# Optimization experiments

Hardware: AMD Instinct MI355X
Metric: run time of the kernel (lower is better)

Reference implementation:

```python
import jax, jax.numpy as jnp
import numpy as np
from jax import lax

B, C, H, W = 8, 128, 256, 256
OUT_CH = 64
IN_CH = C * 9  # 1152: module's in_channels = 9 * image channels (unfold with 3x3 kernel)


def setup_inputs() -> dict:
    key = jax.random.key(0)
    k1, k2, k3 = jax.random.split(key, 3)
    x = jax.random.normal(k1, (B, C, H, W), dtype=jnp.float32)
    style = jax.random.normal(k2, (B, IN_CH), dtype=jnp.float32)
    # learned parameter: torch.randn(out_channels, in_channels, 1, 1) -> store as (out, in)
    weight = jax.random.normal(k3, (OUT_CH, IN_CH), dtype=jnp.float32)
    return {"x": x, "style": style, "weight": weight}


def reference(x, style, weight):
    b, c, h, w = x.shape
    out_ch, in_ch = weight.shape  # in_ch == c * 9
    # unfold column ordering is (c, kh, kw), so the flattened weight is exactly a
    # 3x3 conv kernel: (out, c*9) -> (out, c, 3, 3)
    w33 = weight.reshape(out_ch, c, 3, 3)
    # style.view(B,1,in_ch,1,1) * weight -> per-sample modulated 3x3 kernels
    w_mod = style.reshape(b, 1, c, 3, 3) * w33[None]  # (B, out, c, 3, 3)

    def conv_one(xi, wi):
        # xi: (c, h, w), wi: (out, c, 3, 3); SAME padding matches padding=(1,1)
        return lax.conv_general_dilated(
            xi[None], wi, window_strides=(1, 1), padding="SAME",
            dimension_numbers=("NCHW", "OIHW", "NCHW"))[0]

    out = jax.vmap(conv_one)(x, w_mod)  # (B, out, h, w)
    return out
```

## Files before the change

kernel.cpp:

```cpp
#include <hip/hip_runtime.h>
#include <hip/hip_bf16.h>

#define BATCH 8
#define CIN   128
#define HH    256
#define WW    256
#define OUTC  64
#define INCH  1152
#define HW    (HH*WW)

typedef __attribute__((ext_vector_type(8))) short short8;
typedef __attribute__((ext_vector_type(4))) float f32x4;

__device__ __forceinline__ unsigned short bf16r(float f) {
    unsigned u = __builtin_bit_cast(unsigned, f);
    u += 0x7fffu + ((u >> 16) & 1u);
    return (unsigned short)(u >> 16);
}

__global__ void __launch_bounds__(256) wmod_kernel(const float* __restrict__ weight,
                                                   const float* __restrict__ style,
                                                   unsigned short* __restrict__ wmod) {
    int i = blockIdx.x * 256 + threadIdx.x;
    if (i >= BATCH * 9 * OUTC * CIN) return;
    int c    = i & (CIN - 1);
    int rest = i >> 7;
    int o    = rest & (OUTC - 1);
    int bt   = rest >> 6;
    int tap  = bt % 9;
    int b    = bt / 9;
    int k    = c * 9 + tap;
    float v = weight[o * INCH + k] * style[b * INCH + k];
    wmod[i] = bf16r(v);
}

template <bool GW>
__global__ void __launch_bounds__(512, 4) conv_kernel(
    const float* __restrict__ x,
    const unsigned short* __restrict__ wmod,
    const float* __restrict__ weight,
    const float* __restrict__ style,
    float* __restrict__ out)
{
    __shared__ __align__(16) unsigned short xs_sm[170 * 64];

    const int tid = threadIdx.x;
    const int bx  = blockIdx.x;
    const int b   = blockIdx.y;
    const int h0  = (bx >> 3) * 8;
    const int w0  = (bx & 7) * 32;

    const int wv  = tid >> 6;
    const int wr  = wv >> 2;
    const int wc  = wv & 3;
    const int l15 = tid & 15;
    const int kg  = (tid >> 4) & 3;

    int sbase[4];
#pragma unroll
    for (int ni = 0; ni < 4; ++ni) {
        int p = wc * 64 + ni * 16 + l15;
        sbase[ni] = (p >> 5) * 34 + (p & 31);
    }

    const bool tvalid = tid < 400;
    const int scg = tvalid ? tid / 100 : 0;
    const int srw = tvalid ? tid % 100 : 0;
    const int sr  = srw / 10;
    const int swq = srw % 10;
    const int sh  = h0 - 1 + sr;
    const bool hok = (unsigned)sh < HH;
    const int wload  = w0 - 4 + swq * 4;
    const int wclamp = min(max(wload, 0), WW - 4);
    const int gbase  = (hok ? sh : 0) * WW + wclamp;

    f32x4 acc[2][4];
#pragma unroll
    for (int mi = 0; mi < 2; ++mi)
#pragma unroll
        for (int ni = 0; ni < 4; ++ni) acc[mi][ni] = (f32x4){0.f, 0.f, 0.f, 0.f};

    for (int chunk = 0; chunk < 4; ++chunk) {
        if (chunk) __syncthreads();

        if (tvalid) {
            const float* xp =
                x + ((size_t)(b * CIN + chunk * 32 + scg * 8)) * HW + gbase;
            f32x4 f[8];
#pragma unroll
            for (int j = 0; j < 8; ++j)
                f[j] = hok ? *(const f32x4*)(xp + (size_t)j * HW)
                           : (f32x4){0.f, 0.f, 0.f, 0.f};
#pragma unroll
            for (int u = 0; u < 4; ++u) {
                int w   = wload + u;
                int col = w - (w0 - 1);
                if (col >= 0 && col <= 33) {
                    bool wok = hok && ((unsigned)w < WW);
                    short8 sv;
#pragma unroll
                    for (int j = 0; j < 8; ++j)
                        sv[j] = wok ? (short)bf16r(f[j][u]) : (short)0;
                    int s = sr * 34 + col;
                    int q = s >> 1;
                    int g = (((s & 1) << 2) | scg) ^ (q & 7);
                    *(short8*)&xs_sm[q * 64 + g * 8] = sv;
                }
            }
        }
        __syncthreads();

        const unsigned short* wmb = wmod + ((size_t)(b * 9) * OUTC) * CIN + chunk * 32;
#pragma unroll
        for (int tap = 0; tap < 9; ++tap) {
            const int kh = tap / 3, kw = tap % 3;

            short8 A[2];
            if (GW) {
                const unsigned short* wt = wmb + (size_t)tap * OUTC * CIN;
#pragma unroll
                for (int mi = 0; mi < 2; ++mi)
                    A[mi] = *(const short8*)(wt + (wr * 32 + mi * 16 + l15) * CIN +
                                             kg * 8);
            } else {
#pragma unroll
                for (int mi = 0; mi < 2; ++mi) {
                    int o = wr * 32 + mi * 16 + l15;
#pragma unroll
                    for (int j = 0; j < 8; ++j) {
                        int c = chunk * 32 + kg * 8 + j;
                        int k = c * 9 + tap;
                        A[mi][j] = (short)bf16r(weight[o * INCH + k] *
                                                style[b * INCH + k]);
                    }
                }
            }

            short8 Bv[4];
#pragma unroll
            for (int ni = 0; ni < 4; ++ni) {
                int s = sbase[ni] + kh * 34 + kw;
                int q = s >> 1;
                int g = (((s & 1) << 2) | kg) ^ (q & 7);
                Bv[ni] = *(const short8*)&xs_sm[q * 64 + g * 8];
            }
#pragma unroll
            for (int mi = 0; mi < 2; ++mi)
#pragma unroll
                for (int ni = 0; ni < 4; ++ni)
                    acc[mi][ni] = __builtin_amdgcn_mfma_f32_16x16x32_bf16(
                        A[mi], Bv[ni], acc[mi][ni], 0, 0, 0);
        }
    }

    float* op = out + ((size_t)b * OUTC) * HW;
#pragma unroll
    for (int mi = 0; mi < 2; ++mi) {
#pragma unroll
        for (int ni = 0; ni < 4; ++ni) {
            int p = wc * 64 + ni * 16 + l15;
            int h = h0 + (p >> 5), w = w0 + (p & 31);
#pragma unroll
            for (int r = 0; r < 4; ++r) {
                int o = wr * 32 + mi * 16 + kg * 4 + r;
                op[(size_t)o * HW + h * WW + w] = acc[mi][ni][r];
            }
        }
    }
}

extern "C" void kernel_launch(void* const* d_in, const int* in_sizes, int n_in,
                              void* d_out, int out_size, void* d_ws, size_t ws_size,
                              hipStream_t stream) {
    const float* x      = (const float*)d_in[0];
    const float* style  = (const float*)d_in[1];
    const float* weight = (const float*)d_in[2];
    float* out = (float*)d_out;

    const size_t wmod_bytes = (size_t)BATCH * 9 * OUTC * CIN * sizeof(unsigned short);
    if (ws_size >= wmod_bytes) {
        int total = BATCH * 9 * OUTC * CIN;
        wmod_kernel<<<(total + 255) / 256, 256, 0, stream>>>(weight, style,
                                                             (unsigned short*)d_ws);
        conv_kernel<true><<<dim3(256, BATCH), 512, 0, stream>>>(
            x, (const unsigned short*)d_ws, nullptr, nullptr, out);
    } else {
        conv_kernel<false><<<dim3(256, BATCH), 512, 0, stream>>>(
            x, nullptr, weight, style, out);
    }
}
```

Baseline: 227.4 us.

## Pre-transpose input to NHWC bf16 and double-buffer LDS with async global-to-LDS loads

Result: slower. 327.9 us (+44.2%).

```diff
diff --git a/kernel.cpp b/kernel.cpp
--- a/kernel.cpp
+++ b/kernel.cpp
@@ -9,13 +9,26 @@
 #define INCH  1152
 #define HW    (HH*WW)
 
+#define XT_BYTES   ((size_t)BATCH * HH * WW * CIN * 2)
+#define WMOD_BYTES ((size_t)BATCH * 9 * OUTC * CIN * 2)
+#define ZG_BYTES   16
+
 typedef __attribute__((ext_vector_type(8))) short short8;
 typedef __attribute__((ext_vector_type(4))) float f32x4;
+typedef __attribute__((ext_vector_type(4))) unsigned int u32x4;
 
 __device__ __forceinline__ unsigned short bf16r(float f) {
     unsigned u = __builtin_bit_cast(unsigned, f);
     u += 0x7fffu + ((u >> 16) & 1u);
     return (unsigned short)(u >> 16);
+}
+
+__device__ __forceinline__ void gload_lds16(const unsigned short* src,
+                                            unsigned short* dst_lds) {
+    __builtin_amdgcn_global_load_lds(
+        (const __attribute__((address_space(1))) unsigned int*)(const void*)src,
+        (__attribute__((address_space(3))) unsigned int*)(void*)dst_lds,
+        16, 0, 0);
 }
 
 __global__ void __launch_bounds__(256) wmod_kernel(const float* __restrict__ weight,
@@ -34,6 +47,154 @@
     wmod[i] = bf16r(v);
 }
 
+__global__ void __launch_bounds__(256) transpose_kernel(const float* __restrict__ x,
+                                                        unsigned short* __restrict__ xT) {
+    const int w  = blockIdx.x * 64 + (threadIdx.x & 63);
+    const int c0 = (threadIdx.x >> 6) * 32;
+    const int h  = blockIdx.y;
+    const int b  = blockIdx.z;
+
+    const float* xp = x + ((size_t)(b * CIN + c0)) * HW + h * WW + w;
+    unsigned short* op = xT + ((size_t)(b * HH + h) * WW + w) * CIN + c0;
+
+    float f[32];
+#pragma unroll
+    for (int j = 0; j < 32; ++j) f[j] = xp[(size_t)j * HW];
+
+    unsigned pk[16];
+#pragma unroll
+    for (int j = 0; j < 16; ++j)
+        pk[j] = (unsigned)bf16r(f[2 * j]) | ((unsigned)bf16r(f[2 * j + 1]) << 16);
+
+#pragma unroll
+    for (int u = 0; u < 4; ++u) {
+        u32x4 v = {pk[u * 4 + 0], pk[u * 4 + 1], pk[u * 4 + 2], pk[u * 4 + 3]};
+        *(u32x4*)(op + u * 8) = v;
+    }
+}
+
+__global__ void __launch_bounds__(512, 4) conv2_kernel(
+    const unsigned short* __restrict__ xT,
+    const unsigned short* __restrict__ wmod,
+    const unsigned short* __restrict__ zerog,
+    float* __restrict__ out)
+{
+    __shared__ __align__(16) unsigned short xs_sm[2][170 * 64];
+
+    const int tid = threadIdx.x;
+    const int bx  = blockIdx.x;
+    const int b   = blockIdx.y;
+    const int h0  = (bx >> 3) * 8;
+    const int w0  = (bx & 7) * 32;
+
+    const int wv  = tid >> 6;
+    const int wr  = wv >> 2;
+    const int wc  = wv & 3;
+    const int l15 = tid & 15;
+    const int kg  = (tid >> 4) & 3;
+
+    size_t goff[3];
+    bool   gok[3];
+#pragma unroll
+    for (int i = 0; i < 3; ++i) {
+        int G = tid + i * 512;
+        int Gc = (G < 1360) ? G : 0;
+        int q = Gc >> 3, g = Gc & 7;
+        int pc = g ^ (q & 7);
+        int s  = (q << 1) | (pc >> 2);
+        int cg = pc & 3;
+        int r   = s / 34;
+        int col = s - r * 34;
+        int h = h0 - 1 + r, w = w0 - 1 + col;
+        gok[i]  = ((unsigned)h < HH) && ((unsigned)w < WW);
+        goff[i] = ((size_t)(b * HH + (h & 255)) * WW + (w & 255)) * CIN + cg * 8;
+    }
+
+    int sbase[4];
+#pragma unroll
+    for (int ni = 0; ni < 4; ++ni) {
+        int p = wc * 64 + ni * 16 + l15;
+        sbase[ni] = (p >> 5) * 34 + (p & 31);
+    }
+
+    f32x4 acc[2][4];
+#pragma unroll
+    for (int mi = 0; mi < 2; ++mi)
+#pragma unroll
+        for (int ni = 0; ni < 4; ++ni) acc[mi][ni] = (f32x4){0.f, 0.f, 0.f, 0.f};
+
+    auto stage = [&](int chunk, unsigned short* buf) {
+#pragma unroll
+        for (int i = 0; i < 3; ++i) {
+            if (i < 2 || tid < 336) {
+                const unsigned short* src =
+                    gok[i] ? (xT + goff[i] + chunk * 32) : zerog;
+                unsigned short* dst = buf + (i * 512 + wv * 64) * 8;
+                gload_lds16(src, dst);
+            }
+        }
+    };
+
+    auto compute = [&](int chunk, const unsigned short* xs) {
+        const unsigned short* wmb =
+            wmod + ((size_t)(b * 9) * OUTC) * CIN + chunk * 32;
+#pragma unroll
+        for (int tap = 0; tap < 9; ++tap) {
+            const int kh = tap / 3, kw = tap % 3;
+
+            short8 A[2];
+            const unsigned short* wt = wmb + (size_t)tap * OUTC * CIN;
+#pragma unroll
+            for (int mi = 0; mi < 2; ++mi)
+                A[mi] = *(const short8*)(wt + (wr * 32 + mi * 16 + l15) * CIN +
+                                         kg * 8);
+
+            short8 Bv[4];
+#pragma unroll
+            for (int ni = 0; ni < 4; ++ni) {
+                int s = sbase[ni] + kh * 34 + kw;
+                int q = s >> 1;
+                int g = (((s & 1) << 2) | kg) ^ (q & 7);
+                Bv[ni] = *(const short8*)&xs[q * 64 + g * 8];
+            }
+#pragma unroll
+            for (int mi = 0; mi < 2; ++mi)
+#pragma unroll
+                for (int ni = 0; ni < 4; ++ni)
+                    acc[mi][ni] = __builtin_amdgcn_mfma_f32_16x16x32_bf16(
+                        A[mi], Bv[ni], acc[mi][ni], 0, 0, 0);
+        }
+    };
+
+    stage(0, xs_sm[0]);
+    __syncthreads();
+    stage(1, xs_sm[1]);
+    compute(0, xs_sm[0]);
+    __syncthreads();
+    stage(2, xs_sm[0]);
+    compute(1, xs_sm[1]);
+    __syncthreads();
+    stage(3, xs_sm[1]);
+    compute(2, xs_sm[0]);
+    __syncthreads();
+    compute(3, xs_sm[1]);
+
+    float* op = out + ((size_t)b * OUTC) * HW;
+#pragma unroll
+    for (int mi = 0; mi < 2; ++mi) {
+#pragma unroll
+        for (int ni = 0; ni < 4; ++ni) {
+            int p = wc * 64 + ni * 16 + l15;
+            int h = h0 + (p >> 5), w = w0 + (p & 31);
+#pragma unroll
+            for (int r = 0; r < 4; ++r) {
+                int o = wr * 32 + mi * 16 + kg * 4 + r;
+                op[(size_t)o * HW + h * WW + w] = acc[mi][ni][r];
+            }
+        }
+    }
+}
+
 template <bool GW>
 __global__ void __launch_bounds__(512, 4) conv_kernel(
     const float* __restrict__ x,
@@ -177,13 +338,22 @@
     const float* weight = (const float*)d_in[2];
     float* out = (float*)d_out;
 
-    const size_t wmod_bytes = (size_t)BATCH * 9 * OUTC * CIN * sizeof(unsigned short);
-    if (ws_size >= wmod_bytes) {
-        int total = BATCH * 9 * OUTC * CIN;
-        wmod_kernel<<<(total + 255) / 256, 256, 0, stream>>>(weight, style,
-                                                             (unsigned short*)d_ws);
+    const int wmod_total = BATCH * 9 * OUTC * CIN;
+
+    if (ws_size >= XT_BYTES + WMOD_BYTES + ZG_BYTES) {
+        unsigned short* xT    = (unsigned short*)d_ws;
+        unsigned short* wmodp = (unsigned short*)((char*)d_ws + XT_BYTES);
+        unsigned short* zerog = (unsigned short*)((char*)d_ws + XT_BYTES + WMOD_BYTES);
+
+        wmod_kernel<<<(wmod_total + 255) / 256, 256, 0, stream>>>(weight, style, wmodp);
+        transpose_kernel<<<dim3(4, HH, BATCH), 256, 0, stream>>>(x, xT);
+        hipMemsetAsync(zerog, 0, ZG_BYTES, stream);
+        conv2_kernel<<<dim3(256, BATCH), 512, 0, stream>>>(xT, wmodp, zerog, out);
+    } else if (ws_size >= WMOD_BYTES) {
+        unsigned short* wmodp = (unsigned short*)d_ws;
+        wmod_kernel<<<(wmod_total + 255) / 256, 256, 0, stream>>>(weight, style, wmodp);
         conv_kernel<true><<<dim3(256, BATCH), 512, 0, stream>>>(
-            x, (const unsigned short*)d_ws, nullptr, nullptr, out);
+            x, wmodp, nullptr, nullptr, out);
     } else {
         conv_kernel<false><<<dim3(256, BATCH), 512, 0, stream>>>(
             x, nullptr, weight, style, out);
```

## Shrink conv tiles and double-buffer LDS with register-prefetched input chunks

Applied to the files above, without the earlier changes.

New measurement: 264.3 us. +16.2%, slower.

```diff
diff --git a/kernel.cpp b/kernel.cpp
--- a/kernel.cpp
+++ b/kernel.cpp
@@ -8,9 +8,11 @@
 #define OUTC  64
 #define INCH  1152
 #define HW    (HH*WW)
+#define WMOD_BYTES ((size_t)BATCH * 9 * OUTC * CIN * 2)
 
 typedef __attribute__((ext_vector_type(8))) short short8;
 typedef __attribute__((ext_vector_type(4))) float f32x4;
+typedef __attribute__((ext_vector_type(4), aligned(4))) float f32x4u;
 
 __device__ __forceinline__ unsigned short bf16r(float f) {
     unsigned u = __builtin_bit_cast(unsigned, f);
@@ -30,49 +32,48 @@
     int tap  = bt % 9;
     int b    = bt / 9;
     int k    = c * 9 + tap;
-    float v = weight[o * INCH + k] * style[b * INCH + k];
-    wmod[i] = bf16r(v);
+    wmod[i] = bf16r(weight[o * INCH + k] * style[b * INCH + k]);
 }
 
 template <bool GW>
-__global__ void __launch_bounds__(512, 4) conv_kernel(
+__global__ void __launch_bounds__(128, 2) conv4_kernel(
     const float* __restrict__ x,
     const unsigned short* __restrict__ wmod,
     const float* __restrict__ weight,
     const float* __restrict__ style,
     float* __restrict__ out)
 {
-    __shared__ __align__(16) unsigned short xs_sm[170 * 64];
+    __shared__ __align__(16) unsigned short xs_sm[2][108 * 32];
 
     const int tid = threadIdx.x;
     const int bx  = blockIdx.x;
     const int b   = blockIdx.y;
-    const int h0  = (bx >> 3) * 8;
-    const int w0  = (bx & 7) * 32;
-
-    const int wv  = tid >> 6;
-    const int wr  = wv >> 2;
-    const int wc  = wv & 3;
+    const int h0  = (bx >> 4) * 4;
+    const int w0  = (bx & 15) * 16;
+
+    const int wr  = tid >> 6;
     const int l15 = tid & 15;
     const int kg  = (tid >> 4) & 3;
 
-    int sbase[4];
-#pragma unroll
-    for (int ni = 0; ni < 4; ++ni) {
-        int p = wc * 64 + ni * 16 + l15;
-        sbase[ni] = (p >> 5) * 34 + (p & 31);
+    {
+        short8 z = {0, 0, 0, 0, 0, 0, 0, 0};
+        short8* p = (short8*)&xs_sm[0][0];
+        for (int i = tid; i < 2 * 108 * 32 / 8; i += 128) p[i] = z;
     }
 
-    const bool tvalid = tid < 400;
-    const int scg = tvalid ? tid / 100 : 0;
-    const int srw = tvalid ? tid % 100 : 0;
-    const int sr  = srw / 10;
-    const int swq = srw % 10;
+    const bool tval = tid < 120;
+    const int tt  = tval ? tid : 0;
+    const int cg  = tt / 30;
+    const int rem = tt % 30;
+    const int sr  = rem / 5;
+    const int wq  = rem % 5;
     const int sh  = h0 - 1 + sr;
-    const bool hok = (unsigned)sh < HH;
-    const int wload  = w0 - 4 + swq * 4;
-    const int wclamp = min(max(wload, 0), WW - 4);
-    const int gbase  = (hok ? sh : 0) * WW + wclamp;
+    const bool hok = tval && ((unsigned)sh < HH);
+    const int wl  = w0 - 1 + wq * 4;
+    const int wlc = min(max(wl, 0), WW - 4);
+    const int colbase = wlc - (w0 - 1);
+    const float* xsrc = x + ((size_t)(b * CIN + cg * 8)) * HW +
+                        (hok ? sh : 0) * WW + wlc;
 
     f32x4 acc[2][4];
 #pragma unroll
@@ -80,49 +81,47 @@
 #pragma unroll
         for (int ni = 0; ni < 4; ++ni) acc[mi][ni] = (f32x4){0.f, 0.f, 0.f, 0.f};
 
-    for (int chunk = 0; chunk < 4; ++chunk) {
-        if (chunk) __syncthreads();
-
-        if (tvalid) {
-            const float* xp =
-                x + ((size_t)(b * CIN + chunk * 32 + scg * 8)) * HW + gbase;
-            f32x4 f[8];
+    short8 A[9][2];
+    f32x4  g[8];
+
+    auto stageLoad = [&](int chunk) {
+        if (hok) {
 #pragma unroll
             for (int j = 0; j < 8; ++j)
-                f[j] = hok ? *(const f32x4*)(xp + (size_t)j * HW)
-                           : (f32x4){0.f, 0.f, 0.f, 0.f};
+                g[j] = *(const f32x4u*)(xsrc + (size_t)(chunk * 32 + j) * HW);
+        }
+    };
+
+    auto stageWrite = [&](unsigned short* buf) {
+        if (hok) {
 #pragma unroll
             for (int u = 0; u < 4; ++u) {
-                int w   = wload + u;
-                int col = w - (w0 - 1);
-                if (col >= 0 && col <= 33) {
-                    bool wok = hok && ((unsigned)w < WW);
+                int col = colbase + u;
+                if (col >= 0 && col <= 17) {
+                    int s  = sr * 18 + col;
+                    int gr = cg ^ (s & 3);
                     short8 sv;
 #pragma unroll
-                    for (int j = 0; j < 8; ++j)
-                        sv[j] = wok ? (short)bf16r(f[j][u]) : (short)0;
-                    int s = sr * 34 + col;
-                    int q = s >> 1;
-                    int g = (((s & 1) << 2) | scg) ^ (q & 7);
-                    *(short8*)&xs_sm[q * 64 + g * 8] = sv;
+                    for (int j = 0; j < 8; ++j) sv[j] = (short)bf16r(g[j][u]);
+                    *(short8*)&buf[s * 32 + gr * 8] = sv;
                 }
             }
         }
-        __syncthreads();
-
-        const unsigned short* wmb = wmod + ((size_t)(b * 9) * OUTC) * CIN + chunk * 32;
-#pragma unroll
-        for (int tap = 0; tap < 9; ++tap) {
-            const int kh = tap / 3, kw = tap % 3;
-
-            short8 A[2];
-            if (GW) {
-                const unsigned short* wt = wmb + (size_t)tap * OUTC * CIN;
+    };
+
+    auto loadA = [&](int chunk) {
+        if (GW) {
+            const unsigned short* wb =
+                wmod + ((size_t)(b * 9) * OUTC) * CIN + chunk * 32 + kg * 8;
+#pragma unroll
+            for (int tap = 0; tap < 9; ++tap)
 #pragma unroll
                 for (int mi = 0; mi < 2; ++mi)
-                    A[mi] = *(const short8*)(wt + (wr * 32 + mi * 16 + l15) * CIN +
-                                             kg * 8);
-            } else {
+                    A[tap][mi] = *(const short8*)(
+                        wb + ((size_t)tap * OUTC + wr * 32 + mi * 16 + l15) * CIN);
+        } else {
+#pragma unroll
+            for (int tap = 0; tap < 9; ++tap)
 #pragma unroll
                 for (int mi = 0; mi < 2; ++mi) {
                     int o = wr * 32 + mi * 16 + l15;
@@ -130,43 +129,78 @@
                     for (int j = 0; j < 8; ++j) {
                         int c = chunk * 32 + kg * 8 + j;
                         int k = c * 9 + tap;
-                        A[mi][j] = (short)bf16r(weight[o * INCH + k] *
-                                                style[b * INCH + k]);
+                        A[tap][mi][j] = (short)bf16r(weight[o * INCH + k] *
+                                                     style[b * INCH + k]);
                     }
                 }
+        }
+    };
+
+    auto compute = [&](const unsigned short* buf) {
+#pragma unroll
+        for (int kh = 0; kh < 3; ++kh)
+#pragma unroll
+            for (int kw = 0; kw < 3; ++kw) {
+                const int tap = kh * 3 + kw;
+                short8 Bv[4];
+#pragma unroll
+                for (int ni = 0; ni < 4; ++ni) {
+                    int s  = (ni + kh) * 18 + (l15 + kw);
+                    int gr = kg ^ (s & 3);
+                    Bv[ni] = *(const short8*)&buf[s * 32 + gr * 8];
+                }
+#pragma unroll
+                for (int mi = 0; mi < 2; ++mi)
+#pragma unroll
+                    for (int ni = 0; ni < 4; ++ni)
+                        acc[mi][ni] = __builtin_amdgcn_mfma_f32_16x16x32_bf16(
+                            A[tap][mi], Bv[ni], acc[mi][ni], 0, 0, 0);
             }
-
-            short8 Bv[4];
-#pragma unroll
-            for (int ni = 0; ni < 4; ++ni) {
-                int s = sbase[ni] + kh * 34 + kw;
-                int q = s >> 1;
-                int g = (((s & 1) << 2) | kg) ^ (q & 7);
-                Bv[ni] = *(const short8*)&xs_sm[q * 64 + g * 8];
+    };
+
+    __syncthreads();
+
+    stageLoad(0);
+    loadA(0);
+    stageWrite(xs_sm[0]);
+    __syncthreads();
+
+    stageLoad(1);
+    __builtin_amdgcn_sched_barrier(0);
+    compute(xs_sm[0]);
+    __builtin_amdgcn_sched_barrier(0);
+    loadA(1);
+    stageWrite(xs_sm[1]);
+    __syncthreads();
+
+    stageLoad(2);
+    __builtin_amdgcn_sched_barrier(0);
+    compute(xs_sm[1]);
+    __builtin_amdgcn_sched_barrier(0);
+    loadA(2);
+    stageWrite(xs_sm[0]);
+    __syncthreads();
+
+    stageLoad(3);
+    __builtin_amdgcn_sched_barrier(0);
+    compute(xs_sm[0]);
+    __builtin_amdgcn_sched_barrier(0);
+    loadA(3);
+    stageWrite(xs_sm[1]);
+    __syncthreads();
+
+    compute(xs_sm[1]);
+
+    float* op = out + ((size_t)b * OUTC) * HW + (size_t)h0 * WW + w0 + l15;
+#pragma unroll
+    for (int mi = 0; mi < 2; ++mi)
+#pragma unroll
+        for (int ni = 0; ni < 4; ++ni)
+#pragma unroll
+            for (int rr = 0; rr < 4; ++rr) {
+                int o = wr * 32 + mi * 16 + kg * 4 + rr;
+                op[(size_t)o * HW + ni * WW] = acc[mi][ni][rr];
             }
-#pragma unroll
-            for (int mi = 0; mi < 2; ++mi)
-#pragma unroll
-                for (int ni = 0; ni < 4; ++ni)
-                    acc[mi][ni] = __builtin_amdgcn_mfma_f32_16x16x32_bf16(
-                        A[mi], Bv[ni], acc[mi][ni], 0, 0, 0);
-        }
-    }
-
-    float* op = out + ((size_t)b * OUTC) * HW;
-#pragma unroll
-    for (int mi = 0; mi < 2; ++mi) {
-#pragma unroll
-        for (int ni = 0; ni < 4; ++ni) {
-            int p = wc * 64 + ni * 16 + l15;
-            int h = h0 + (p >> 5), w = w0 + (p & 31);
-#pragma unroll
-            for (int r = 0; r < 4; ++r) {
-                int o = wr * 32 + mi * 16 + kg * 4 + r;
-                op[(size_t)o * HW + h * WW + w] = acc[mi][ni][r];
-            }
-        }
-    }
 }
 
 extern "C" void kernel_launch(void* const* d_in, const int* in_sizes, int n_in,
@@ -177,15 +211,15 @@
     const float* weight = (const float*)d_in[2];
     float* out = (float*)d_out;
 
-    const size_t wmod_bytes = (size_t)BATCH * 9 * OUTC * CIN * sizeof(unsigned short);
-    if (ws_size >= wmod_bytes) {
-        int total = BATCH * 9 * OUTC * CIN;
-        wmod_kernel<<<(total + 255) / 256, 256, 0, stream>>>(weight, style,
-                                                             (unsigned short*)d_ws);
-        conv_kernel<true><<<dim3(256, BATCH), 512, 0, stream>>>(
-            x, (const unsigned short*)d_ws, nullptr, nullptr, out);
+    const int wmod_total = BATCH * 9 * OUTC * CIN;
+
+    if (ws_size >= WMOD_BYTES) {
+        unsigned short* wmodp = (unsigned short*)d_ws;
+        wmod_kernel<<<(wmod_total + 255) / 256, 256, 0, stream>>>(weight, style, wmodp);
+        conv4_kernel<true><<<dim3(1024, BATCH), 128, 0, stream>>>(
+            x, wmodp, nullptr, nullptr, out);
     } else {
-        conv_kernel<false><<<dim3(256, BATCH), 512, 0, stream>>>(
+        conv4_kernel<false><<<dim3(1024, BATCH), 128, 0, stream>>>(
             x, nullptr, weight, style, out);
     }
 }
```
